# Kernel tuning notes

Measured on AMD Instinct MI355X. Metric: run time of the kernel, lower is better.

Reference implementation:

```python
import jax, jax.numpy as jnp
import numpy as np

B, T, I, H = 256, 256, 2048, 128

def setup_inputs() -> dict:
    key = jax.random.key(0)
    ks = jax.random.split(key, 7)
    s = 1.0 / np.sqrt(H)  # torch RNN/Linear init scale
    return {
        "x": jax.random.normal(ks[0], (B, T, I), dtype=jnp.float32),
        "W_ih": jax.random.uniform(ks[1], (H, I), jnp.float32, -s, s),
        "W_hh": jax.random.uniform(ks[2], (H, H), jnp.float32, -s, s),
        "b_ih": jax.random.uniform(ks[3], (H,), jnp.float32, -s, s),
        "b_hh": jax.random.uniform(ks[4], (H,), jnp.float32, -s, s),
        "W_fc": jax.random.uniform(ks[5], (1, H), jnp.float32, -s, s),
        "b_fc": jax.random.uniform(ks[6], (1,), jnp.float32, -s, s),
    }

def reference(x, W_ih, W_hh, b_ih, b_hh, W_fc, b_fc):
    # Precompute input projection for all timesteps as one big GEMM: [B,T,H]
    xp = jnp.einsum('bti,hi->bth', x, W_ih) + (b_ih + b_hh)
    h0 = jnp.zeros((x.shape[0], W_hh.shape[0]), dtype=x.dtype)

    def step(h, xt):  # xt: [B,H]
        h = jnp.tanh(xt + h @ W_hh.T)
        return h, None

    hT, _ = jax.lax.scan(step, h0, jnp.swapaxes(xp, 0, 1))  # final hidden [B,H]
    out = hT @ W_fc.T + b_fc  # [B,1]
    return out.squeeze(1)     # [B]
```

## Files before the change

### kernel.cpp

```cpp
#include <hip/hip_runtime.h>
#include <hip/hip_bf16.h>
#include <math.h>

#define B_ 256
#define T_ 256
#define I_ 2048
#define H_ 128

#define BM 64
#define BK 64
#define NKT (I_ / BK)

typedef __attribute__((ext_vector_type(8))) short bf16x8;
typedef __attribute__((ext_vector_type(4))) float f32x4;
typedef _Float16 half2v __attribute__((ext_vector_type(2)));

static __device__ inline short f2bf(float f) {
    __hip_bfloat16 h = __float2bfloat16(f);
    return *reinterpret_cast<short*>(&h);
}

static __device__ inline bf16x8 pack8(float4 a, float4 b) {
    bf16x8 r;
    r[0] = f2bf(a.x); r[1] = f2bf(a.y); r[2] = f2bf(a.z); r[3] = f2bf(a.w);
    r[4] = f2bf(b.x); r[5] = f2bf(b.y); r[6] = f2bf(b.z); r[7] = f2bf(b.w);
    return r;
}

#define LGKM_BARRIER() do {                                  \
    asm volatile("s_waitcnt lgkmcnt(0)" ::: "memory");       \
    __builtin_amdgcn_sched_barrier(0);                       \
    __builtin_amdgcn_s_barrier();                            \
} while (0)

__global__ __launch_bounds__(256) void convW(
    const float* __restrict__ W, short* __restrict__ Wb)
{
    const int g = blockIdx.x * 256 + threadIdx.x;
    const float4 v0 = reinterpret_cast<const float4*>(W)[2 * g];
    const float4 v1 = reinterpret_cast<const float4*>(W)[2 * g + 1];
    reinterpret_cast<bf16x8*>(Wb)[g] = pack8(v0, v1);
}

__global__ __launch_bounds__(256, 2) void proj_mfma(
    const float* __restrict__ x, const short* __restrict__ Wb,
    const float* __restrict__ bih, const float* __restrict__ bhh,
    float* __restrict__ xp)
{
    __shared__ __align__(16) float As[2][BM * BK];
    __shared__ __align__(16) short Bs[2][H_ * BK];

    const int tid  = threadIdx.x;
    const int lane = tid & 63;
    const int wid  = tid >> 6;
    const long row0 = (long)blockIdx.x * BM;

    const int fr = lane & 15;
    const int fq = lane >> 4;

    float biasr[2];
    #pragma unroll
    for (int n = 0; n < 2; ++n) {
        const int col = wid * 32 + n * 16 + fr;
        biasr[n] = bih[col] + bhh[col];
    }

    const int arow_l = lane >> 4;
    const int brow_l = lane >> 3;

    auto STAGE = [&](int tt, int buf) {
        const int kk = tt * BK;
        #pragma unroll
        for (int i = 0; i < 4; ++i) {
            const int r = (wid * 4 + i) * 4 + arow_l;
            const int u = (lane & 15) ^ (r & 15);
            const float* ga = x + (row0 + r) * I_ + kk + u * 4;
            __builtin_amdgcn_global_load_lds(
                (const __attribute__((address_space(1))) void*)ga,
                (__attribute__((address_space(3))) void*)&As[buf][(wid * 4 + i) * 256],
                16, 0, 0);
        }
        #pragma unroll
        for (int i = 0; i < 4; ++i) {
            const int r = (wid * 4 + i) * 8 + brow_l;
            const int u = (lane & 7) ^ (r & 7);
            const short* gb = Wb + (long)r * I_ + kk + u * 8;
            __builtin_amdgcn_global_load_lds(
                (const __attribute__((address_space(1))) void*)gb,
                (__attribute__((address_space(3))) void*)&Bs[buf][(wid * 4 + i) * 512],
                16, 0, 0);
        }
    };

    f32x4 acc[4][2];
    #pragma unroll
    for (int m = 0; m < 4; ++m)
        #pragma unroll
        for (int n = 0; n < 2; ++n)
            acc[m][n] = (f32x4){0.f, 0.f, 0.f, 0.f};

    STAGE(0, 0);
    __syncthreads();

    int p = 0;
    for (int t = 0; t < NKT; ++t) {
        if (t + 1 < NKT) STAGE(t + 1, p ^ 1);

        bf16x8 af[4][2], bfr[2][2];
        #pragma unroll
        for (int m = 0; m < 4; ++m) {
            const int R = m * 16 + fr;
            #pragma unroll
            for (int kk = 0; kk < 2; ++kk) {
                const int U0 = kk * 8 + fq * 2;
                const float4 a0 = *reinterpret_cast<const float4*>(
                    &As[p][R * 64 + ((U0 ^ (R & 15)) << 2)]);
                const float4 a1 = *reinterpret_cast<const float4*>(
                    &As[p][R * 64 + (((U0 + 1) ^ (R & 15)) << 2)]);
                af[m][kk] = pack8(a0, a1);
            }
        }
        #pragma unroll
        for (int n = 0; n < 2; ++n) {
            const int R = wid * 32 + n * 16 + fr;
            #pragma unroll
            for (int kk = 0; kk < 2; ++kk) {
                const int U = kk * 4 + fq;
                bfr[n][kk] = *reinterpret_cast<const bf16x8*>(
                    &Bs[p][R * 64 + ((U ^ (R & 7)) << 3)]);
            }
        }
        #pragma unroll
        for (int kk = 0; kk < 2; ++kk)
            #pragma unroll
            for (int m = 0; m < 4; ++m)
                #pragma unroll
                for (int n = 0; n < 2; ++n)
                    acc[m][n] = __builtin_amdgcn_mfma_f32_16x16x32_bf16(
                        af[m][kk], bfr[n][kk], acc[m][n], 0, 0, 0);

        __syncthreads();
        p ^= 1;
    }

    #pragma unroll
    for (int n = 0; n < 2; ++n) {
        const int col = wid * 32 + n * 16 + fr;
        #pragma unroll
        for (int m = 0; m < 4; ++m) {
            const long rbase = row0 + m * 16 + fq * 4;
            #pragma unroll
            for (int j = 0; j < 4; ++j)
                xp[(rbase + j) * H_ + col] = acc[m][n][j] + biasr[n];
        }
    }
}

__global__ __launch_bounds__(256) void scan_kernel(
    const float* __restrict__ xp, const float* __restrict__ Whh,
    const float* __restrict__ Wfc, const float* __restrict__ bfc,
    float* __restrict__ out)
{
    __shared__ __align__(16) unsigned hpk[2][H_ / 2];

    const int tid  = threadIdx.x;
    const int lane = tid & 63;
    const int w    = tid >> 6;
    const int j    = w * 32 + (lane & 31);
    const int g    = lane >> 5;
    const int b    = blockIdx.x;

    half2v Wh[32];
    {
        const float4* wp = reinterpret_cast<const float4*>(&Whh[(long)j * H_ + g * 64]);
        #pragma unroll
        for (int q = 0; q < 16; ++q) {
            const float4 wv = wp[q];
            half2v p0, p1;
            p0[0] = (_Float16)wv.x; p0[1] = (_Float16)wv.y;
            p1[0] = (_Float16)wv.z; p1[1] = (_Float16)wv.w;
            Wh[2 * q]     = p0;
            Wh[2 * q + 1] = p1;
        }
    }
    if (tid < H_ / 2) hpk[0][tid] = 0u;

    const float* xprow = xp + (long)b * T_ * H_ + j;
    float xa = xprow[0 * H_];
    float xb = xprow[1 * H_];
    float xc = xprow[2 * H_];
    float xd = xprow[3 * H_];
    __syncthreads();

    auto body = [&](int t, float xpv) {
        const uint4* hp = reinterpret_cast<const uint4*>(&hpk[t & 1][g * 32]);
        float a0 = 0.f, a1 = 0.f, a2 = 0.f, a3 = 0.f;
        #pragma unroll
        for (int q = 0; q < 8; ++q) {
            const uint4 u = hp[q];
            a0 = __builtin_amdgcn_fdot2(__builtin_bit_cast(half2v, u.x), Wh[4*q+0], a0, false);
            a1 = __builtin_amdgcn_fdot2(__builtin_bit_cast(half2v, u.y), Wh[4*q+1], a1, false);
            a2 = __builtin_amdgcn_fdot2(__builtin_bit_cast(half2v, u.z), Wh[4*q+2], a2, false);
            a3 = __builtin_amdgcn_fdot2(__builtin_bit_cast(half2v, u.w), Wh[4*q+3], a3, false);
        }
        float part = (a0 + a1) + (a2 + a3);
        part += __shfl_xor(part, 32);
        const float pre = part + xpv;
        const float e = __expf(2.f * pre);
        const float h = 1.f - 2.f / (e + 1.f);
        if (g == 0) {
            reinterpret_cast<unsigned short*>(&hpk[(t + 1) & 1][0])[j] =
                __builtin_bit_cast(unsigned short, (_Float16)h);
        }
        LGKM_BARRIER();
    };

    for (int t = 0; t < T_; t += 4) {
        float xu;
        xu = xa; if (t + 4 < T_) xa = xprow[(long)(t + 4) * H_];
        body(t + 0, xu);
        xu = xb; if (t + 5 < T_) xb = xprow[(long)(t + 5) * H_];
        body(t + 1, xu);
        xu = xc; if (t + 6 < T_) xc = xprow[(long)(t + 6) * H_];
        body(t + 2, xu);
        xu = xd; if (t + 7 < T_) xd = xprow[(long)(t + 7) * H_];
        body(t + 3, xu);
    }

    if (w == 0) {
        const unsigned u = hpk[0][lane];
        const half2v hh = __builtin_bit_cast(half2v, u);
        float v = (float)hh[0] * Wfc[2 * lane] + (float)hh[1] * Wfc[2 * lane + 1];
        #pragma unroll
        for (int off = 32; off > 0; off >>= 1) v += __shfl_down(v, off);
        if (lane == 0) out[b] = v + bfc[0];
    }
}

extern "C" void kernel_launch(void* const* d_in, const int* in_sizes, int n_in,
                              void* d_out, int out_size, void* d_ws, size_t ws_size,
                              hipStream_t stream)
{
    const float* x   = (const float*)d_in[0];
    const float* Wih = (const float*)d_in[1];
    const float* Whh = (const float*)d_in[2];
    const float* bih = (const float*)d_in[3];
    const float* bhh = (const float*)d_in[4];
    const float* Wfc = (const float*)d_in[5];
    const float* bfc = (const float*)d_in[6];
    float* out = (float*)d_out;
    float* xp  = (float*)d_ws;
    short* Wb  = (short*)((char*)d_ws + (size_t)B_ * T_ * H_ * sizeof(float));

    convW<<<dim3((H_ * I_) / (256 * 8)), dim3(256), 0, stream>>>(Wih, Wb);
    proj_mfma<<<dim3((B_ * T_) / BM), dim3(256), 0, stream>>>(x, Wb, bih, bhh, xp);
    scan_kernel<<<dim3(B_), dim3(256), 0, stream>>>(xp, Whh, Wfc, bfc, out);
}
```

Baseline: 232.5 us.

## Load bf16 weight fragments directly to registers, drop LDS B tile, raise occupancy

Removes the shared-memory staging buffer for the bf16 W_ih tile. Each wave now reads its B fragments straight from global memory into a double-buffered register set, prefetched one K-step ahead. The A-fragment conversion is interleaved with the MFMAs, and launch bounds are raised to 4 blocks per CU since LDS use halves. This cuts LDS traffic and footprint at the cost of more register pressure and uncoalesced global weight loads that depend on L2 hits.

```diff
diff --git a/kernel.cpp b/kernel.cpp
--- a/kernel.cpp
+++ b/kernel.cpp
@@ -42,13 +42,12 @@
     reinterpret_cast<bf16x8*>(Wb)[g] = pack8(v0, v1);
 }
 
-__global__ __launch_bounds__(256, 2) void proj_mfma(
+__global__ __launch_bounds__(256, 4) void proj_mfma(
     const float* __restrict__ x, const short* __restrict__ Wb,
     const float* __restrict__ bih, const float* __restrict__ bhh,
     float* __restrict__ xp)
 {
     __shared__ __align__(16) float As[2][BM * BK];
-    __shared__ __align__(16) short Bs[2][H_ * BK];
 
     const int tid  = threadIdx.x;
     const int lane = tid & 63;
@@ -66,7 +65,6 @@
     }
 
     const int arow_l = lane >> 4;
-    const int brow_l = lane >> 3;
 
     auto STAGE = [&](int tt, int buf) {
         const int kk = tt * BK;
@@ -80,15 +78,16 @@
                 (__attribute__((address_space(3))) void*)&As[buf][(wid * 4 + i) * 256],
                 16, 0, 0);
         }
-        #pragma unroll
-        for (int i = 0; i < 4; ++i) {
-            const int r = (wid * 4 + i) * 8 + brow_l;
-            const int u = (lane & 7) ^ (r & 7);
-            const short* gb = Wb + (long)r * I_ + kk + u * 8;
-            __builtin_amdgcn_global_load_lds(
-                (const __attribute__((address_space(1))) void*)gb,
-                (__attribute__((address_space(3))) void*)&Bs[buf][(wid * 4 + i) * 512],
-                16, 0, 0);
+    };
+
+    auto LOADB = [&](int tt, bf16x8 bc[2][2]) {
+        #pragma unroll
+        for (int n = 0; n < 2; ++n) {
+            const int R = wid * 32 + n * 16 + fr;
+            #pragma unroll
+            for (int kk = 0; kk < 2; ++kk)
+                bc[n][kk] = *reinterpret_cast<const bf16x8*>(
+                    Wb + (long)R * I_ + tt * BK + kk * 32 + fq * 8);
         }
     };
 
@@ -99,48 +98,38 @@
         for (int n = 0; n < 2; ++n)
             acc[m][n] = (f32x4){0.f, 0.f, 0.f, 0.f};
 
+    bf16x8 bcA[2][2], bcB[2][2];
+
     STAGE(0, 0);
+    LOADB(0, bcA);
     __syncthreads();
 
-    int p = 0;
-    for (int t = 0; t < NKT; ++t) {
+    auto body = [&](int t, bf16x8 bcur[2][2], bf16x8 bnext[2][2], int p) {
         if (t + 1 < NKT) STAGE(t + 1, p ^ 1);
-
-        bf16x8 af[4][2], bfr[2][2];
-        #pragma unroll
-        for (int m = 0; m < 4; ++m) {
-            const int R = m * 16 + fr;
+        #pragma unroll
+        for (int kk = 0; kk < 2; ++kk) {
             #pragma unroll
-            for (int kk = 0; kk < 2; ++kk) {
+            for (int m = 0; m < 4; ++m) {
+                const int R  = m * 16 + fr;
                 const int U0 = kk * 8 + fq * 2;
                 const float4 a0 = *reinterpret_cast<const float4*>(
                     &As[p][R * 64 + ((U0 ^ (R & 15)) << 2)]);
                 const float4 a1 = *reinterpret_cast<const float4*>(
                     &As[p][R * 64 + (((U0 + 1) ^ (R & 15)) << 2)]);
-                af[m][kk] = pack8(a0, a1);
+                const bf16x8 af = pack8(a0, a1);
+                acc[m][0] = __builtin_amdgcn_mfma_f32_16x16x32_bf16(
+                    af, bcur[0][kk], acc[m][0], 0, 0, 0);
+                acc[m][1] = __builtin_amdgcn_mfma_f32_16x16x32_bf16(
+                    af, bcur[1][kk], acc[m][1], 0, 0, 0);
             }
         }
-        #pragma unroll
-        for (int n = 0; n < 2; ++n) {
-            const int R = wid * 32 + n * 16 + fr;
-            #pragma unroll
-            for (int kk = 0; kk < 2; ++kk) {
-                const int U = kk * 4 + fq;
-                bfr[n][kk] = *reinterpret_cast<const bf16x8*>(
-                    &Bs[p][R * 64 + ((U ^ (R & 7)) << 3)]);
-            }
-        }
-        #pragma unroll
-        for (int kk = 0; kk < 2; ++kk)
-            #pragma unroll
-            for (int m = 0; m < 4; ++m)
-                #pragma unroll
-                for (int n = 0; n < 2; ++n)
-                    acc[m][n] = __builtin_amdgcn_mfma_f32_16x16x32_bf16(
-                        af[m][kk], bfr[n][kk], acc[m][n], 0, 0, 0);
-
+        if (t + 1 < NKT) LOADB(t + 1, bnext);
         __syncthreads();
-        p ^= 1;
+    };
+
+    for (int t = 0; t < NKT; t += 2) {
+        body(t,     bcA, bcB, 0);
+        body(t + 1, bcB, bcA, 1);
     }
 
     #pragma unroll
```

After: 231.0 us. No clear change (-0.6%).
